# Kernel tuning notes

Hardware: AMD Instinct MI355X
Metric: run time of the kernel (lower is better)

## Reference

```python
import jax, jax.numpy as jnp
import numpy as np

B = 1048576
VEC_SZ = 4
LUT_BITS = 8
K = 2 ** LUT_BITS  # 256 codewords


def setup_inputs() -> dict:
    key = jax.random.key(0)
    kx, kt = jax.random.split(key)
    X = jax.random.normal(kx, (B, VEC_SZ), dtype=jnp.float32)
    tlut = jax.random.normal(kt, (K, VEC_SZ), dtype=jnp.float32)  # codebook [K, vec_sz]
    return {"X": X, "tlut": tlut}


def reference(X, tlut):
    # torch.cdist(X, tlut) -> argmin is equivalent to argmin of squared distances:
    x_sq = jnp.sum(X * X, axis=-1, keepdims=True)            # [B, 1]
    c_sq = jnp.sum(tlut * tlut, axis=-1)                     # [K]
    cross = jnp.einsum('bd,kd->bk', X, tlut)                 # [B, K]
    dist2 = x_sq - 2.0 * cross + c_sq                        # [B, K]
    state = jnp.argmin(dist2, axis=-1).astype(jnp.int32)     # [B]
    hatX = jnp.take(tlut, state, axis=0)                     # gather reconstruction [B, vec_sz]
    return hatX, state
```

## Files before the change

### kernel.cpp

```cpp
#include <hip/hip_runtime.h>

#define K_CW 256
#define PPT 4
#define KHALF 128

__global__ void vq_csq_kernel(const float* __restrict__ tlut, float* __restrict__ csq) {
    int k = threadIdx.x;
    float c0 = tlut[k * 4 + 0];
    float c1 = tlut[k * 4 + 1];
    float c2 = tlut[k * 4 + 2];
    float c3 = tlut[k * 4 + 3];
    float s = __fadd_rn(__fadd_rn(__fadd_rn(__fmul_rn(c0, c0), __fmul_rn(c1, c1)),
                                  __fmul_rn(c2, c2)),
                        __fmul_rn(c3, c3));
    csq[k] = s;
}

__global__ __launch_bounds__(512) void vq_argmin_kernel(
    const float* __restrict__ X,
    const float* __restrict__ tlut,
    const float* __restrict__ csq,
    float* __restrict__ outX,
    float* __restrict__ outS,
    int B) {
    __shared__ float4 sd[256];
    __shared__ int4   si[256];

    const int t = threadIdx.x;
    const int tt = t & 255;
    const int half = t >> 8;
    const int kbase = __builtin_amdgcn_readfirstlane(half << 7);

    const int g = blockIdx.x * 256 + tt;
    const int stride = B / PPT;

    const float4* __restrict__ X4 = reinterpret_cast<const float4*>(X);
    const float4* __restrict__ T4 = reinterpret_cast<const float4*>(tlut);

    float x0[PPT], x1[PPT], x2[PPT], x3[PPT], xsq[PPT], bestd[PPT];
    int besti[PPT];

    #pragma unroll
    for (int i = 0; i < PPT; ++i) {
        const float4 xv = X4[g + i * stride];
        x0[i] = xv.x; x1[i] = xv.y; x2[i] = xv.z; x3[i] = xv.w;
        xsq[i] = __fadd_rn(__fadd_rn(__fadd_rn(__fmul_rn(xv.x, xv.x), __fmul_rn(xv.y, xv.y)),
                                     __fmul_rn(xv.z, xv.z)),
                           __fmul_rn(xv.w, xv.w));
        bestd[i] = __builtin_inff();
        besti[i] = kbase;
    }

    #pragma unroll 8
    for (int kk = 0; kk < KHALF; ++kk) {
        const int k = kbase + kk;
        const float4 c = T4[k];
        const float cs = csq[k];
        #pragma unroll
        for (int i = 0; i < PPT; ++i) {
            float cross = __fmul_rn(x0[i], c.x);
            cross = __fmaf_rn(x1[i], c.y, cross);
            cross = __fmaf_rn(x2[i], c.z, cross);
            cross = __fmaf_rn(x3[i], c.w, cross);
            float t2 = __fmaf_rn(-2.0f, cross, xsq[i]);
            float d = __fadd_rn(t2, cs);
            besti[i] = (d < bestd[i]) ? k : besti[i];
            bestd[i] = fminf(d, bestd[i]);
        }
    }

    if (half == 1) {
        sd[tt] = make_float4(bestd[0], bestd[1], bestd[2], bestd[3]);
        si[tt] = make_int4(besti[0], besti[1], besti[2], besti[3]);
    }
    __syncthreads();
    if (half == 0) {
        const float4 od = sd[tt];
        const int4   oi = si[tt];
        if (od.x < bestd[0]) { bestd[0] = od.x; besti[0] = oi.x; }
        if (od.y < bestd[1]) { bestd[1] = od.y; besti[1] = oi.y; }
        if (od.z < bestd[2]) { bestd[2] = od.z; besti[2] = oi.z; }
        if (od.w < bestd[3]) { bestd[3] = od.w; besti[3] = oi.w; }

        #pragma unroll
        for (int i = 0; i < PPT; ++i) {
            const int p = g + i * stride;
            reinterpret_cast<float4*>(outX)[p] = T4[besti[i]];
            outS[p] = (float)besti[i];
        }
    }
}

extern "C" void kernel_launch(void* const* d_in, const int* in_sizes, int n_in,
                              void* d_out, int out_size, void* d_ws, size_t ws_size,
                              hipStream_t stream) {
    const float* X    = (const float*)d_in[0];
    const float* tlut = (const float*)d_in[1];
    const int B = in_sizes[0] / 4;

    float* outX = (float*)d_out;
    float* outS = outX + (size_t)B * 4;

    float* csq = (float*)d_ws;

    vq_csq_kernel<<<1, 256, 0, stream>>>(tlut, csq);

    const int groups = B / PPT;
    const int grid = groups / 256;
    vq_argmin_kernel<<<grid, 512, 0, stream>>>(X, tlut, csq, outX, outS, B);
}
```

Baseline: 116.2 us.

## Split codebook search four ways per point and pack codeword with its norm

Each block now uses 1024 threads, with four groups of 256 threads each scanning a quarter of the codebook for the same points, followed by a three-way shared-memory reduction. A prep kernel packs each codeword with its squared norm into a 32-byte record, so one load replaces two separate loads. This shortens each thread's serial argmin chain and gives more waves per point set for latency hiding. The cost is a larger reduction, more shared memory, and extra padding bytes in the packed table.

```diff
diff --git a/kernel.cpp b/kernel.cpp
--- a/kernel.cpp
+++ b/kernel.cpp
@@ -2,9 +2,12 @@
 
 #define K_CW 256
 #define PPT 4
-#define KHALF 128
+#define NQ 4
+#define KQ (K_CW / NQ)
 
-__global__ void vq_csq_kernel(const float* __restrict__ tlut, float* __restrict__ csq) {
+struct P8 { float4 a; float4 b; };
+
+__global__ void vq_pack_kernel(const float* __restrict__ tlut, float* __restrict__ pk) {
     int k = threadIdx.x;
     float c0 = tlut[k * 4 + 0];
     float c1 = tlut[k * 4 + 1];
@@ -13,29 +16,31 @@
     float s = __fadd_rn(__fadd_rn(__fadd_rn(__fmul_rn(c0, c0), __fmul_rn(c1, c1)),
                                   __fmul_rn(c2, c2)),
                         __fmul_rn(c3, c3));
-    csq[k] = s;
+    pk[k * 8 + 0] = c0; pk[k * 8 + 1] = c1; pk[k * 8 + 2] = c2; pk[k * 8 + 3] = c3;
+    pk[k * 8 + 4] = s;  pk[k * 8 + 5] = 0.f; pk[k * 8 + 6] = 0.f; pk[k * 8 + 7] = 0.f;
 }
 
-__global__ __launch_bounds__(512) void vq_argmin_kernel(
+__global__ __launch_bounds__(1024, 8) void vq_argmin_kernel(
     const float* __restrict__ X,
     const float* __restrict__ tlut,
-    const float* __restrict__ csq,
+    const float* __restrict__ pk,
     float* __restrict__ outX,
     float* __restrict__ outS,
     int B) {
-    __shared__ float4 sd[256];
-    __shared__ int4   si[256];
+    __shared__ float4 sd[3 * 256];
+    __shared__ int4   si[3 * 256];
 
     const int t = threadIdx.x;
     const int tt = t & 255;
-    const int half = t >> 8;
-    const int kbase = __builtin_amdgcn_readfirstlane(half << 7);
+    const int q = t >> 8;
+    const int kbase = __builtin_amdgcn_readfirstlane(q << 6);
 
     const int g = blockIdx.x * 256 + tt;
     const int stride = B / PPT;
 
     const float4* __restrict__ X4 = reinterpret_cast<const float4*>(X);
     const float4* __restrict__ T4 = reinterpret_cast<const float4*>(tlut);
+    const P8* __restrict__ PK = reinterpret_cast<const P8*>(pk);
 
     float x0[PPT], x1[PPT], x2[PPT], x3[PPT], xsq[PPT], bestd[PPT];
     int besti[PPT];
@@ -51,11 +56,12 @@
         besti[i] = kbase;
     }
 
-    #pragma unroll 8
-    for (int kk = 0; kk < KHALF; ++kk) {
+    #pragma unroll 16
+    for (int kk = 0; kk < KQ; ++kk) {
         const int k = kbase + kk;
-        const float4 c = T4[k];
-        const float cs = csq[k];
+        const P8 e = PK[k];
+        const float4 c = e.a;
+        const float cs = e.b.x;
         #pragma unroll
         for (int i = 0; i < PPT; ++i) {
             float cross = __fmul_rn(x0[i], c.x);
@@ -69,19 +75,21 @@
         }
     }
 
-    if (half == 1) {
-        sd[tt] = make_float4(bestd[0], bestd[1], bestd[2], bestd[3]);
-        si[tt] = make_int4(besti[0], besti[1], besti[2], besti[3]);
+    if (q > 0) {
+        sd[(q - 1) * 256 + tt] = make_float4(bestd[0], bestd[1], bestd[2], bestd[3]);
+        si[(q - 1) * 256 + tt] = make_int4(besti[0], besti[1], besti[2], besti[3]);
     }
     __syncthreads();
-    if (half == 0) {
-        const float4 od = sd[tt];
-        const int4   oi = si[tt];
-        if (od.x < bestd[0]) { bestd[0] = od.x; besti[0] = oi.x; }
-        if (od.y < bestd[1]) { bestd[1] = od.y; besti[1] = oi.y; }
-        if (od.z < bestd[2]) { bestd[2] = od.z; besti[2] = oi.z; }
-        if (od.w < bestd[3]) { bestd[3] = od.w; besti[3] = oi.w; }
-
+    if (q == 0) {
+        #pragma unroll
+        for (int j = 0; j < 3; ++j) {
+            const float4 od = sd[j * 256 + tt];
+            const int4   oi = si[j * 256 + tt];
+            if (od.x < bestd[0]) { bestd[0] = od.x; besti[0] = oi.x; }
+            if (od.y < bestd[1]) { bestd[1] = od.y; besti[1] = oi.y; }
+            if (od.z < bestd[2]) { bestd[2] = od.z; besti[2] = oi.z; }
+            if (od.w < bestd[3]) { bestd[3] = od.w; besti[3] = oi.w; }
+        }
         #pragma unroll
         for (int i = 0; i < PPT; ++i) {
             const int p = g + i * stride;
@@ -101,11 +109,11 @@
     float* outX = (float*)d_out;
     float* outS = outX + (size_t)B * 4;
 
-    float* csq = (float*)d_ws;
+    float* pk = (float*)d_ws;
 
-    vq_csq_kernel<<<1, 256, 0, stream>>>(tlut, csq);
+    vq_pack_kernel<<<1, 256, 0, stream>>>(tlut, pk);
 
     const int groups = B / PPT;
     const int grid = groups / 256;
-    vq_argmin_kernel<<<grid, 512, 0, stream>>>(X, tlut, csq, outX, outS, B);
+    vq_argmin_kernel<<<grid, 1024, 0, stream>>>(X, tlut, pk, outX, outS, B);
 }
```

Result: no change. 115.5 us (-0.6%).
